# Performance work log

Measured on AMD Instinct MI355X. Metric: run time of the kernel, lower is better.

Reference implementation:

```python
import jax, jax.numpy as jnp
import numpy as np

EPS = 1e-12  # tf.nn.l2_normalize epsilon used inside keras CosineSimilarity


def _cos(a, b):
    # keras CosineSimilarity returns -cos; callers negate explicitly.
    an = a / jnp.sqrt(jnp.maximum(jnp.sum(a * a, axis=-1, keepdims=True), EPS))
    bn = b / jnp.sqrt(jnp.maximum(jnp.sum(b * b, axis=-1, keepdims=True), EPS))
    return jnp.sum(an * bn, axis=-1)


def setup_inputs() -> dict:
    key = jax.random.key(0)
    B, S, D, H, N = 1024, 200, 128, 128, 64
    ks = jax.random.split(key, 8)
    X_series = jax.random.normal(ks[0], (B, S, D), jnp.float32)
    pos_series = jax.random.normal(ks[1], (S, D), jnp.float32)
    X_item = jax.random.normal(ks[2], (B, D), jnp.float32)
    origin = jax.random.normal(ks[3], (B, N, D), jnp.float32)  # X_negative
    # contiguous-prefix validity mask (module assumes valid positions form a prefix)
    lengths = jax.random.randint(ks[4], (B,), 1, S + 1)
    valid_mask = jnp.arange(S)[None, :] < lengths[:, None]
    # learned params (GlorotUniform-scale init)
    Wp = jax.random.normal(ks[5], (D, H), jnp.float32) * 0.08
    We = jax.random.normal(ks[6], (D, H), jnp.float32) * 0.08
    z = jax.random.normal(ks[7], (H,), jnp.float32) * 0.1
    return {"X_series": X_series, "pos_series": pos_series, "X_item": X_item,
            "valid_mask": valid_mask, "origin": origin, "Wp": Wp, "We": We, "z": z}


def reference(X_series, pos_series, X_item, valid_mask, origin, Wp, We, z):
    B, S, D = X_series.shape
    # additive tanh attention: z . tanh(X_series @ We + pos_series @ Wp)
    hidden = jnp.tanh(jnp.einsum('bsd,dh->bsh', X_series, We) + (pos_series @ Wp)[None])
    scores = jnp.einsum('bsh,h->bs', hidden, z)
    scores = jnp.where(valid_mask, scores, -jnp.inf)
    attn = jax.nn.softmax(scores, axis=-1)                      # [B,S]
    attentioned = attn[:, :, None] * X_series                    # [B,S,D]
    attention_output = jnp.sum(attentioned, axis=1)              # [B,D]
    inner = jnp.sum(attention_output * X_item, axis=-1, keepdims=True)
    concated = jnp.concatenate([attention_output, inner], axis=1)  # [B,D+1]

    # ---- auxiliary loss ----
    last_idx = jnp.sum(valid_mask.astype(jnp.int32), axis=1) - 1
    last_vec = attentioned[jnp.arange(B), last_idx]              # gather_nd
    new_mask = (jnp.arange(S)[None, :] < last_idx[:, None]).astype(X_series.dtype)
    out_vec = jnp.sum(attentioned * new_mask[:, :, None], axis=1)  # [B,D]
    # keras CosineSimilarity = -cos_sim; then mapped to (x+1)/2 and used as logits
    pos_logits = (-_cos(last_vec, out_vec) + 1.0) / 2.0          # [B]
    neg_logits = (-_cos(origin, out_vec[:, None, :]) + 1.0) / 2.0  # [B,N]
    pos_loss = jax.nn.softplus(-pos_logits)  # sigmoid_xent labels=1
    neg_loss = jax.nn.softplus(neg_logits)   # sigmoid_xent labels=0
    # NB: TF reduces pos_loss over its only axis -> scalar, broadcast-added to [B]
    auxiliary_loss = jnp.sum(pos_loss) + jnp.sum(neg_loss, axis=-1)  # [B]
    return concated, auxiliary_loss
```

## Files before the change

### kernel.cpp

```cpp
#include <hip/hip_runtime.h>
#include <hip/hip_bf16.h>
#include <math.h>

#define B_ 1024
#define S_ 200
#define D_ 128
#define H_ 128
#define N_ 64

typedef __attribute__((ext_vector_type(8))) short short8;
typedef __attribute__((ext_vector_type(8))) __bf16 bf16x8;
typedef __attribute__((ext_vector_type(4))) float floatx4;

static __device__ __forceinline__ float bf2f(unsigned short u) {
    union { unsigned int i; float f; } v; v.i = ((unsigned int)u) << 16; return v.f;
}
static __device__ __forceinline__ unsigned short f2bf(float f) {
    union { float f; unsigned int u; } v; v.f = f;
    unsigned int u = v.u;
    return (unsigned short)((u + 0x7FFFu + ((u >> 16) & 1u)) >> 16);
}
static __device__ __forceinline__ float ld1(const void* p, int isbf, size_t i) {
    return isbf ? bf2f(((const unsigned short*)p)[i]) : ((const float*)p)[i];
}
static __device__ __forceinline__ float fast_tanh(float x) {
    float t = __expf(2.0f * x);
    return 1.0f - 2.0f * __builtin_amdgcn_rcpf(t + 1.0f);
}

__global__ __launch_bounds__(64) void detect_kernel(
    const void* a0, const void* a1, const void* a2, const void* a3,
    const void* a4, const void* a5, const void* a6, const void* a7,
    int* flags)
{
    int bid = blockIdx.x, t = threadIdx.x;
    if (bid == 3) {
        const unsigned char* mb = (const unsigned char*)a3;
        int f = 0;
        for (int i = t; i < 4096; i += 64)
            if ((i & 3) && mb[i]) f = 1;
        for (int off = 32; off; off >>= 1) f |= __shfl_xor(f, off, 64);
        if (t == 0) flags[3] = f;
        return;
    }
    const void* ptrs[8] = {a0, a1, a2, a3, a4, a5, a6, a7};
    const int counts[8] = {B_*S_*D_, S_*D_, B_*D_, 0, B_*N_*D_, D_*H_, D_*H_, H_};
    const unsigned int* w = (const unsigned int*)ptrs[bid];
    int words = counts[bid] / 2; if (words > 1024) words = 1024;
    int pass = 0, tot = 0;
    for (int i = t; i < words; i += 64) {
        unsigned int e = (w[i] >> 7) & 0xFF;
        tot++;
        if (e == 0 || (e >= 96 && e <= 140)) pass++;
    }
    for (int off = 32; off; off >>= 1) {
        pass += __shfl_xor(pass, off, 64);
        tot  += __shfl_xor(tot,  off, 64);
    }
    if (t == 0) flags[bid] = (pass * 4 >= tot * 3) ? 1 : 0;
}

__global__ __launch_bounds__(256) void lengths_kernel(
    const void* __restrict__ maskv, const int* __restrict__ flags,
    int* __restrict__ lengths)
{
    int wv = threadIdx.x >> 6, lane = threadIdx.x & 63;
    int fMk = flags[3];
    int base = blockIdx.x * 64 + wv * 16;
    for (int bb = 0; bb < 16; ++bb) {
        int b = base + bb;
        int nz = 0;
        if (fMk) {
            const unsigned char* mb = (const unsigned char*)maskv + (size_t)b * S_;
            for (int i = lane; i < S_; i += 64) nz += (mb[i] != 0);
        } else {
            const int* mi = (const int*)maskv + (size_t)b * S_;
            for (int i = lane; i < S_; i += 64) nz += (mi[i] != 0);
        }
        for (int off = 32; off; off >>= 1) nz += __shfl_xor(nz, off, 64);
        if (lane == 0) lengths[b] = nz;
    }
}

__global__ __launch_bounds__(128) void prep_kernel(
    const void* __restrict__ We, const void* __restrict__ pos,
    const void* __restrict__ Wp, const int* __restrict__ flags,
    unsigned short* __restrict__ WeTf, float* __restrict__ pb)
{
    int blk = blockIdx.x, t = threadIdx.x;
    __shared__ unsigned short T[128][136];
    __shared__ float prow[D_];
    if (blk == 0) {
        int fWe = flags[6];
        for (int c = t; c < 2048; c += 128) {
            int d = c >> 4, h8 = (c & 15) * 8;
            short8 v;
            if (fWe) {
                v = *(const short8*)((const unsigned short*)We + d * H_ + h8);
            } else {
                const float* p = (const float*)We + d * H_ + h8;
                float4 a = ((const float4*)p)[0], b = ((const float4*)p)[1];
                v[0] = (short)f2bf(a.x); v[1] = (short)f2bf(a.y);
                v[2] = (short)f2bf(a.z); v[3] = (short)f2bf(a.w);
                v[4] = (short)f2bf(b.x); v[5] = (short)f2bf(b.y);
                v[6] = (short)f2bf(b.z); v[7] = (short)f2bf(b.w);
            }
            *(short8*)(&T[d][h8]) = v;
        }
        __syncthreads();
        for (int i = t; i < 2048; i += 128) {
            int frag = i >> 6, ln = i & 63;
            int nt = frag >> 2, kks = frag & 3;
            int h = nt * 16 + (ln & 15);
            int dbase = kks * 32 + (ln >> 4) * 8;
            short8 v;
#pragma unroll
            for (int j = 0; j < 8; ++j) v[j] = (short)T[dbase + j][h];
            *(short8*)(WeTf + (size_t)i * 8) = v;
        }
    } else {
        int s = blk - 1, h = t;
        prow[h] = ld1(pos, flags[1], (size_t)s * D_ + h);
        __syncthreads();
        float acc = 0.f;
        if (flags[5]) {
            const unsigned short* W = (const unsigned short*)Wp;
            for (int d = 0; d < D_; ++d) acc = fmaf(prow[d], bf2f(W[d * H_ + h]), acc);
        } else {
            const float* W = (const float*)Wp;
            for (int d = 0; d < D_; ++d) acc = fmaf(prow[d], W[d * H_ + h], acc);
        }
        pb[s * H_ + h] = acc;
    }
}

__global__ __launch_bounds__(256) void scores_kernel(
    const void* __restrict__ Xs, const unsigned short* __restrict__ WeTf,
    const void* __restrict__ zv, const float* __restrict__ pb,
    const int* __restrict__ flags, const int* __restrict__ lengths,
    float* __restrict__ scores)
{
    __shared__ unsigned short Bsh[16384];
    int t = threadIdx.x;
    int lane = t & 63, w = t >> 6;
    int quad = lane >> 4, mrow = lane & 15;
    int fXs = flags[0], fz = flags[7];
    int row0 = blockIdx.x * 128 + w * 32;

    for (int i = t; i < 2048; i += 256)
        *(short8*)(Bsh + i * 8) = *(const short8*)(WeTf + (size_t)i * 8);

    float zl[8];
#pragma unroll
    for (int nt = 0; nt < 8; ++nt) zl[nt] = ld1(zv, fz, nt * 16 + mrow);
    __syncthreads();

#pragma unroll
    for (int mt = 0; mt < 2; ++mt) {
        int r = row0 + mt * 16 + mrow;
        int bidx = r / S_, s_ = r - bidx * S_;
        bool valid = s_ < lengths[bidx];
        if (!__any(valid)) continue;

        floatx4 acc[8];
#pragma unroll
        for (int nt = 0; nt < 8; ++nt) {
            acc[nt][0] = 0.f; acc[nt][1] = 0.f; acc[nt][2] = 0.f; acc[nt][3] = 0.f;
        }
#pragma unroll
        for (int kks = 0; kks < 4; ++kks) {
            bf16x8 af;
            size_t roff = (size_t)r * D_ + kks * 32 + quad * 8;
            if (fXs) {
                short8 v = *(const short8*)((const unsigned short*)Xs + roff);
                af = __builtin_bit_cast(bf16x8, v);
            } else {
                const float* p = (const float*)Xs + roff;
                float4 a = ((const float4*)p)[0], b = ((const float4*)p)[1];
                short8 v;
                v[0] = (short)f2bf(a.x); v[1] = (short)f2bf(a.y);
                v[2] = (short)f2bf(a.z); v[3] = (short)f2bf(a.w);
                v[4] = (short)f2bf(b.x); v[5] = (short)f2bf(b.y);
                v[6] = (short)f2bf(b.z); v[7] = (short)f2bf(b.w);
                af = __builtin_bit_cast(bf16x8, v);
            }
#pragma unroll
            for (int nt = 0; nt < 8; ++nt) {
                short8 bv = *(const short8*)(Bsh + (((nt << 2) + kks) * 64 + lane) * 8);
                bf16x8 bf = __builtin_bit_cast(bf16x8, bv);
                acc[nt] = __builtin_amdgcn_mfma_f32_16x16x32_bf16(af, bf, acc[nt], 0, 0, 0);
            }
        }
#pragma unroll
        for (int reg = 0; reg < 4; ++reg) {
            int grow = row0 + mt * 16 + quad * 4 + reg;
            int s = grow % S_;
            const float* pbrow = pb + (size_t)s * H_;
            float rs = 0.f;
#pragma unroll
            for (int nt = 0; nt < 8; ++nt)
                rs = fmaf(fast_tanh(acc[nt][reg] + pbrow[nt * 16 + mrow]), zl[nt], rs);
#pragma unroll
            for (int off = 1; off < 16; off <<= 1)
                rs += __shfl_xor(rs, off, 64);
            if (mrow == 0) scores[grow] = rs;
        }
    }
}

__global__ __launch_bounds__(256) void attnout_kernel(
    const void* __restrict__ Xs, const void* __restrict__ Xitem,
    const void* __restrict__ origin, const float* __restrict__ scores,
    const int* __restrict__ flags, const int* __restrict__ lengths,
    float* __restrict__ pos_loss, float* __restrict__ neg_sum,
    float* __restrict__ out)
{
    int b = blockIdx.x, t = threadIdx.x;
    int wv = t >> 6, lane = t & 63;
    int fXs = flags[0], fXi = flags[2], fOr = flags[4];
    __shared__ float attn[256];
    __shared__ float att_out[D_];
    __shared__ float lastv[D_];
    __shared__ float outv[D_];
    __shared__ float partial[8][D_];
    __shared__ float p_oo[4][64];
    __shared__ float p_ov[4][64];
    __shared__ float red[16];
    __shared__ float sc1s, sc2s, vvs;

    int nn = t >> 2, part = t & 3;
    float o_f[32];
    if (fOr) {
        const unsigned short* p = (const unsigned short*)origin + ((size_t)b * N_ + nn) * D_ + part * 32;
#pragma unroll
        for (int j = 0; j < 4; ++j) {
            uint4 u = *(const uint4*)(p + j * 8);
            o_f[j*8+0] = bf2f((unsigned short)(u.x & 0xffff));
            o_f[j*8+1] = bf2f((unsigned short)(u.x >> 16));
            o_f[j*8+2] = bf2f((unsigned short)(u.y & 0xffff));
            o_f[j*8+3] = bf2f((unsigned short)(u.y >> 16));
            o_f[j*8+4] = bf2f((unsigned short)(u.z & 0xffff));
            o_f[j*8+5] = bf2f((unsigned short)(u.z >> 16));
            o_f[j*8+6] = bf2f((unsigned short)(u.w & 0xffff));
            o_f[j*8+7] = bf2f((unsigned short)(u.w >> 16));
        }
    } else {
        const float* p = (const float*)origin + ((size_t)b * N_ + nn) * D_ + part * 32;
#pragma unroll
        for (int j = 0; j < 8; ++j) {
            float4 v = *(const float4*)(p + j * 4);
            o_f[j*4+0] = v.x; o_f[j*4+1] = v.y; o_f[j*4+2] = v.z; o_f[j*4+3] = v.w;
        }
    }

    int length = lengths[b];
    int last = length - 1;

    float sc = (t < length) ? scores[(size_t)b * S_ + t] : -INFINITY;
    float m = sc;
    for (int off = 32; off; off >>= 1) m = fmaxf(m, __shfl_xor(m, off, 64));
    if (lane == 0) red[wv] = m;
    __syncthreads();
    if (t == 0) sc1s = fmaxf(fmaxf(red[0], red[1]), fmaxf(red[2], red[3]));
    __syncthreads();
    float e = (t < length) ? expf(sc - sc1s) : 0.f;
    float r = e;
    for (int off = 32; off; off >>= 1) r += __shfl_xor(r, off, 64);
    __syncthreads();
    if (lane == 0) red[wv] = r;
    __syncthreads();
    if (t == 0) sc2s = red[0] + red[1] + red[2] + red[3];
    __syncthreads();
    attn[t] = e / sc2s;
    __syncthreads();

    {
        int sp = t >> 5;
        int d4 = (t & 31) * 4;
        float a0 = 0, a1 = 0, a2 = 0, a3 = 0;
        if (fXs) {
#pragma unroll 5
            for (int s = sp; s < length; s += 8) {
                float ww = attn[s];
                uint2 u = *(const uint2*)((const unsigned short*)Xs + ((size_t)b * S_ + s) * D_ + d4);
                a0 = fmaf(ww, bf2f((unsigned short)(u.x & 0xffff)), a0);
                a1 = fmaf(ww, bf2f((unsigned short)(u.x >> 16)), a1);
                a2 = fmaf(ww, bf2f((unsigned short)(u.y & 0xffff)), a2);
                a3 = fmaf(ww, bf2f((unsigned short)(u.y >> 16)), a3);
            }
        } else {
#pragma unroll 5
            for (int s = sp; s < length; s += 8) {
                float ww = attn[s];
                float4 u = *(const float4*)((const float*)Xs + ((size_t)b * S_ + s) * D_ + d4);
                a0 = fmaf(ww, u.x, a0);
                a1 = fmaf(ww, u.y, a1);
                a2 = fmaf(ww, u.z, a2);
                a3 = fmaf(ww, u.w, a3);
            }
        }
        partial[sp][d4] = a0; partial[sp][d4 + 1] = a1;
        partial[sp][d4 + 2] = a2; partial[sp][d4 + 3] = a3;
    }
    __syncthreads();
    if (t < D_) {
        float v = 0.f;
#pragma unroll
        for (int p = 0; p < 8; ++p) v += partial[p][t];
        att_out[t] = v;
        float lv = attn[last] * ld1(Xs, fXs, ((size_t)b * S_ + last) * D_ + t);
        lastv[t] = lv;
        outv[t] = v - lv;
    }
    __syncthreads();

    {
        float pi = (t < D_) ? att_out[t] * ld1(Xitem, fXi, (size_t)b * D_ + t) : 0.f;
        for (int off = 32; off; off >>= 1) pi += __shfl_xor(pi, off, 64);
        if (lane == 0) red[wv] = pi;
        __syncthreads();
        if (t < D_) out[(size_t)b * (D_ + 1) + t] = att_out[t];
        if (t == 0)
            out[(size_t)b * (D_ + 1) + D_] = red[0] + red[1] + red[2] + red[3];
        __syncthreads();
    }

    {
        float l_ = (t < D_) ? lastv[t] : 0.f;
        float o_ = (t < D_) ? outv[t] : 0.f;
        float r0 = l_ * l_, r1 = l_ * o_, r2 = o_ * o_;
        for (int off = 32; off; off >>= 1) {
            r0 += __shfl_xor(r0, off, 64);
            r1 += __shfl_xor(r1, off, 64);
            r2 += __shfl_xor(r2, off, 64);
        }
        if (lane == 0) { red[wv] = r0; red[4 + wv] = r1; red[8 + wv] = r2; }
        __syncthreads();
        if (t == 0) {
            float ll = red[0] + red[1] + red[2] + red[3];
            float lo = red[4] + red[5] + red[6] + red[7];
            float oo = red[8] + red[9] + red[10] + red[11];
            float cosv = lo / (sqrtf(fmaxf(ll, 1e-12f)) * sqrtf(fmaxf(oo, 1e-12f)));
            float pl = 0.5f * (1.f - cosv);
            pos_loss[b] = log1pf(expf(-pl));
            vvs = oo;
        }
        __syncthreads();
    }

    {
        float o_oo = 0.f, o_ov = 0.f;
#pragma unroll
        for (int jj = 0; jj < 32; ++jj) {
            int j = (jj + part * 8) & 31;
            float wv_ = outv[part * 32 + j];
            o_oo = fmaf(o_f[j], o_f[j], o_oo);
            o_ov = fmaf(o_f[j], wv_, o_ov);
        }
        p_oo[part][nn] = o_oo;
        p_ov[part][nn] = o_ov;
        __syncthreads();
        if (t < 64) {
            float oo = p_oo[0][t] + p_oo[1][t] + p_oo[2][t] + p_oo[3][t];
            float ov = p_ov[0][t] + p_ov[1][t] + p_ov[2][t] + p_ov[3][t];
            float cosn = ov / (sqrtf(fmaxf(oo, 1e-12f)) * sqrtf(fmaxf(vvs, 1e-12f)));
            float nl = 0.5f * (1.f - cosn);
            float nloss = log1pf(expf(nl));
            for (int off = 32; off; off >>= 1) nloss += __shfl_xor(nloss, off, 64);
            if (t == 0) neg_sum[b] = nloss;
        }
    }
}

__global__ __launch_bounds__(1024) void final_kernel(
    const float* __restrict__ pos_loss,
    const float* __restrict__ neg_sum,
    float* __restrict__ out)
{
    __shared__ float red[16];
    int t = threadIdx.x;
    float v = pos_loss[t];
    for (int off = 32; off; off >>= 1) v += __shfl_xor(v, off, 64);
    if ((t & 63) == 0) red[t >> 6] = v;
    __syncthreads();
    if (t == 0) {
        float s = 0.f;
#pragma unroll
        for (int i = 0; i < 16; ++i) s += red[i];
        red[0] = s;
    }
    __syncthreads();
    out[(size_t)B_ * (D_ + 1) + t] = red[0] + neg_sum[t];
}

extern "C" void kernel_launch(void* const* d_in, const int* in_sizes, int n_in,
                              void* d_out, int out_size, void* d_ws, size_t ws_size,
                              hipStream_t stream) {
    const void* Xs     = d_in[0];
    const void* pos    = d_in[1];
    const void* Xitem  = d_in[2];
    const void* mask   = d_in[3];
    const void* origin = d_in[4];
    const void* Wp     = d_in[5];
    const void* We     = d_in[6];
    const void* zv     = d_in[7];

    int*   flags    = (int*)d_ws;
    unsigned short* WeTf = (unsigned short*)((char*)d_ws + 128);
    float* pb       = (float*)((char*)d_ws + 128 + 32768);
    float* scores   = pb + 25600;
    float* pos_loss = scores + 204800;
    float* neg_sum  = pos_loss + B_;
    int*   lengths  = (int*)(neg_sum + B_);
    float* out = (float*)d_out;

    detect_kernel<<<8, 64, 0, stream>>>(Xs, pos, Xitem, mask, origin, Wp, We, zv, flags);
    lengths_kernel<<<16, 256, 0, stream>>>(mask, flags, lengths);
    prep_kernel<<<201, 128, 0, stream>>>(We, pos, Wp, flags, WeTf, pb);
    scores_kernel<<<(B_ * S_) / 128, 256, 0, stream>>>(Xs, WeTf, zv, pb, flags, lengths, scores);
    attnout_kernel<<<B_, 256, 0, stream>>>(Xs, Xitem, origin, scores, flags, lengths,
                                           pos_loss, neg_sum, out);
    final_kernel<<<1, 1024, 0, stream>>>(pos_loss, neg_sum, out);
}
```

Before: 280.9 us.

## Merge detect/lengths/prep kernels and interleave two MFMA row tiles in scores

Fuses the dtype-detect, lengths and prep kernels into one launch. Each block recomputes the flags it needs locally instead of waiting for a separate detect launch. The scores kernel now exits whole blocks early when every row lies past the valid length, before staging weights in LDS. It also issues two independent MFMA accumulator chains per wave so A-loads and MFMAs can overlap. The cost is redundant detection work per block and higher register pressure from doubled accumulators.

```diff
diff --git a/kernel.cpp b/kernel.cpp
--- a/kernel.cpp
+++ b/kernel.cpp
@@ -27,28 +27,9 @@
     float t = __expf(2.0f * x);
     return 1.0f - 2.0f * __builtin_amdgcn_rcpf(t + 1.0f);
 }
-
-__global__ __launch_bounds__(64) void detect_kernel(
-    const void* a0, const void* a1, const void* a2, const void* a3,
-    const void* a4, const void* a5, const void* a6, const void* a7,
-    int* flags)
-{
-    int bid = blockIdx.x, t = threadIdx.x;
-    if (bid == 3) {
-        const unsigned char* mb = (const unsigned char*)a3;
-        int f = 0;
-        for (int i = t; i < 4096; i += 64)
-            if ((i & 3) && mb[i]) f = 1;
-        for (int off = 32; off; off >>= 1) f |= __shfl_xor(f, off, 64);
-        if (t == 0) flags[3] = f;
-        return;
-    }
-    const void* ptrs[8] = {a0, a1, a2, a3, a4, a5, a6, a7};
-    const int counts[8] = {B_*S_*D_, S_*D_, B_*D_, 0, B_*N_*D_, D_*H_, D_*H_, H_};
-    const unsigned int* w = (const unsigned int*)ptrs[bid];
-    int words = counts[bid] / 2; if (words > 1024) words = 1024;
+static __device__ __forceinline__ int detect_bf16_wave(const unsigned int* w, int words, int lane) {
     int pass = 0, tot = 0;
-    for (int i = t; i < words; i += 64) {
+    for (int i = lane; i < words; i += 64) {
         unsigned int e = (w[i] >> 7) & 0xFF;
         tot++;
         if (e == 0 || (e >= 96 && e <= 140)) pass++;
@@ -57,41 +38,78 @@
         pass += __shfl_xor(pass, off, 64);
         tot  += __shfl_xor(tot,  off, 64);
     }
-    if (t == 0) flags[bid] = (pass * 4 >= tot * 3) ? 1 : 0;
-}
-
-__global__ __launch_bounds__(256) void lengths_kernel(
-    const void* __restrict__ maskv, const int* __restrict__ flags,
-    int* __restrict__ lengths)
-{
-    int wv = threadIdx.x >> 6, lane = threadIdx.x & 63;
-    int fMk = flags[3];
-    int base = blockIdx.x * 64 + wv * 16;
-    for (int bb = 0; bb < 16; ++bb) {
-        int b = base + bb;
-        int nz = 0;
-        if (fMk) {
-            const unsigned char* mb = (const unsigned char*)maskv + (size_t)b * S_;
-            for (int i = lane; i < S_; i += 64) nz += (mb[i] != 0);
-        } else {
-            const int* mi = (const int*)maskv + (size_t)b * S_;
-            for (int i = lane; i < S_; i += 64) nz += (mi[i] != 0);
-        }
-        for (int off = 32; off; off >>= 1) nz += __shfl_xor(nz, off, 64);
-        if (lane == 0) lengths[b] = nz;
-    }
-}
-
-__global__ __launch_bounds__(128) void prep_kernel(
-    const void* __restrict__ We, const void* __restrict__ pos,
-    const void* __restrict__ Wp, const int* __restrict__ flags,
-    unsigned short* __restrict__ WeTf, float* __restrict__ pb)
+    return (pass * 4 >= tot * 3) ? 1 : 0;
+}
+
+__global__ __launch_bounds__(128) void prep_all_kernel(
+    const void* __restrict__ Xs, const void* __restrict__ pos,
+    const void* __restrict__ Xitem, const void* __restrict__ maskv,
+    const void* __restrict__ origin, const void* __restrict__ Wp,
+    const void* __restrict__ We, const void* __restrict__ zv,
+    int* __restrict__ flags, unsigned short* __restrict__ WeTf,
+    float* __restrict__ pb, int* __restrict__ lengths)
 {
     int blk = blockIdx.x, t = threadIdx.x;
-    __shared__ unsigned short T[128][136];
-    __shared__ float prow[D_];
-    if (blk == 0) {
-        int fWe = flags[6];
+    int lane = t & 63;
+
+    if (blk < 8) {
+        if (t >= 64) return;
+        if (blk == 3) {
+            const unsigned char* mb = (const unsigned char*)maskv;
+            int f = 0;
+            for (int i = t; i < 4096; i += 64)
+                if ((i & 3) && mb[i]) f = 1;
+            for (int off = 32; off; off >>= 1) f |= __shfl_xor(f, off, 64);
+            if (t == 0) flags[3] = f;
+            return;
+        }
+        const void* ptrs[8] = {Xs, pos, Xitem, maskv, origin, Wp, We, zv};
+        const int counts[8] = {B_*S_*D_, S_*D_, B_*D_, 0, B_*N_*D_, D_*H_, D_*H_, H_};
+        int words = counts[blk] / 2; if (words > 1024) words = 1024;
+        int r = detect_bf16_wave((const unsigned int*)ptrs[blk], words, t);
+        if (t == 0) flags[blk] = r;
+        return;
+    }
+
+    if (blk < 40) {
+        __shared__ int fMk_s;
+        const unsigned char* mb = (const unsigned char*)maskv;
+        if (t < 64) {
+            int f = 0;
+            for (int i = t; i < 4096; i += 64)
+                if ((i & 3) && mb[i]) f = 1;
+            for (int off = 32; off; off >>= 1) f |= __shfl_xor(f, off, 64);
+            if (t == 0) fMk_s = f;
+        }
+        __syncthreads();
+        int fMk = fMk_s;
+        int wv = t >> 6;
+        int base = (blk - 8) * 32 + wv * 16;
+        for (int bb = 0; bb < 16; ++bb) {
+            int b = base + bb;
+            int nz = 0;
+            if (fMk) {
+                const unsigned char* mp = mb + (size_t)b * S_;
+                for (int i = lane; i < S_; i += 64) nz += (mp[i] != 0);
+            } else {
+                const int* mi = (const int*)maskv + (size_t)b * S_;
+                for (int i = lane; i < S_; i += 64) nz += (mi[i] != 0);
+            }
+            for (int off = 32; off; off >>= 1) nz += __shfl_xor(nz, off, 64);
+            if (lane == 0) lengths[b] = nz;
+        }
+        return;
+    }
+
+    if (blk == 40) {
+        __shared__ unsigned short T[128][136];
+        __shared__ int fWe_s;
+        if (t < 64) {
+            int r = detect_bf16_wave((const unsigned int*)We, 1024, t);
+            if (t == 0) fWe_s = r;
+        }
+        __syncthreads();
+        int fWe = fWe_s;
         for (int c = t; c < 2048; c += 128) {
             int d = c >> 4, h8 = (c & 15) * 8;
             short8 v;
@@ -118,12 +136,23 @@
             for (int j = 0; j < 8; ++j) v[j] = (short)T[dbase + j][h];
             *(short8*)(WeTf + (size_t)i * 8) = v;
         }
-    } else {
-        int s = blk - 1, h = t;
-        prow[h] = ld1(pos, flags[1], (size_t)s * D_ + h);
+        return;
+    }
+
+    {
+        __shared__ float prow[D_];
+        __shared__ int f2[2];
+        if (t < 64) {
+            int rp = detect_bf16_wave((const unsigned int*)pos, 1024, t);
+            int rw = detect_bf16_wave((const unsigned int*)Wp, 1024, t);
+            if (t == 0) { f2[0] = rp; f2[1] = rw; }
+        }
+        __syncthreads();
+        int s = blk - 41, h = t;
+        prow[h] = ld1(pos, f2[0], (size_t)s * D_ + h);
         __syncthreads();
         float acc = 0.f;
-        if (flags[5]) {
+        if (f2[1]) {
             const unsigned short* W = (const unsigned short*)Wp;
             for (int d = 0; d < D_; ++d) acc = fmaf(prow[d], bf2f(W[d * H_ + h]), acc);
         } else {
@@ -145,7 +174,13 @@
     int lane = t & 63, w = t >> 6;
     int quad = lane >> 4, mrow = lane & 15;
     int fXs = flags[0], fz = flags[7];
-    int row0 = blockIdx.x * 128 + w * 32;
+    int rb = blockIdx.x * 128;
+
+    {
+        int bidx = rb / S_, s0 = rb - bidx * S_;
+        bool crosses = (s0 + 127 >= S_);
+        if (!crosses && s0 >= lengths[bidx]) return;
+    }
 
     for (int i = t; i < 2048; i += 256)
         *(short8*)(Bsh + i * 8) = *(const short8*)(WeTf + (size_t)i * 8);
@@ -155,56 +190,88 @@
     for (int nt = 0; nt < 8; ++nt) zl[nt] = ld1(zv, fz, nt * 16 + mrow);
     __syncthreads();
 
+    int row0 = rb + w * 32;
+    bool v[2];
 #pragma unroll
     for (int mt = 0; mt < 2; ++mt) {
-        int r = row0 + mt * 16 + mrow;
-        int bidx = r / S_, s_ = r - bidx * S_;
-        bool valid = s_ < lengths[bidx];
-        if (!__any(valid)) continue;
-
-        floatx4 acc[8];
-#pragma unroll
-        for (int nt = 0; nt < 8; ++nt) {
-            acc[nt][0] = 0.f; acc[nt][1] = 0.f; acc[nt][2] = 0.f; acc[nt][3] = 0.f;
-        }
+        int rf = row0 + mt * 16;
+        int bidx = rf / S_, s0 = rf - bidx * S_;
+        v[mt] = (s0 + 15 >= S_) || (s0 < lengths[bidx]);
+    }
+    if (!v[0] && !v[1]) return;
+
+    floatx4 accA[8], accB[8];
+#pragma unroll
+    for (int nt = 0; nt < 8; ++nt) {
+        accA[nt][0] = 0.f; accA[nt][1] = 0.f; accA[nt][2] = 0.f; accA[nt][3] = 0.f;
+        accB[nt][0] = 0.f; accB[nt][1] = 0.f; accB[nt][2] = 0.f; accB[nt][3] = 0.f;
+    }
+
+    auto loadA = [&](int r, int kks) -> bf16x8 {
+        size_t roff = (size_t)r * D_ + kks * 32 + quad * 8;
+        if (fXs) {
+            short8 vv = *(const short8*)((const unsigned short*)Xs + roff);
+            return __builtin_bit_cast(bf16x8, vv);
+        }
+        const float* p = (const float*)Xs + roff;
+        float4 a = ((const float4*)p)[0], b = ((const float4*)p)[1];
+        short8 vv;
+        vv[0] = (short)f2bf(a.x); vv[1] = (short)f2bf(a.y);
+        vv[2] = (short)f2bf(a.z); vv[3] = (short)f2bf(a.w);
+        vv[4] = (short)f2bf(b.x); vv[5] = (short)f2bf(b.y);
+        vv[6] = (short)f2bf(b.z); vv[7] = (short)f2bf(b.w);
+        return __builtin_bit_cast(bf16x8, vv);
+    };
+
+    int mtv = v[0] ? 0 : 1;
+    if (v[0] && v[1]) {
+        int r0 = row0 + mrow, r1 = row0 + 16 + mrow;
 #pragma unroll
         for (int kks = 0; kks < 4; ++kks) {
-            bf16x8 af;
-            size_t roff = (size_t)r * D_ + kks * 32 + quad * 8;
-            if (fXs) {
-                short8 v = *(const short8*)((const unsigned short*)Xs + roff);
-                af = __builtin_bit_cast(bf16x8, v);
-            } else {
-                const float* p = (const float*)Xs + roff;
-                float4 a = ((const float4*)p)[0], b = ((const float4*)p)[1];
-                short8 v;
-                v[0] = (short)f2bf(a.x); v[1] = (short)f2bf(a.y);
-                v[2] = (short)f2bf(a.z); v[3] = (short)f2bf(a.w);
-                v[4] = (short)f2bf(b.x); v[5] = (short)f2bf(b.y);
-                v[6] = (short)f2bf(b.z); v[7] = (short)f2bf(b.w);
-                af = __builtin_bit_cast(bf16x8, v);
-            }
+            bf16x8 a0 = loadA(r0, kks), a1 = loadA(r1, kks);
 #pragma unroll
             for (int nt = 0; nt < 8; ++nt) {
                 short8 bv = *(const short8*)(Bsh + (((nt << 2) + kks) * 64 + lane) * 8);
                 bf16x8 bf = __builtin_bit_cast(bf16x8, bv);
-                acc[nt] = __builtin_amdgcn_mfma_f32_16x16x32_bf16(af, bf, acc[nt], 0, 0, 0);
-            }
-        }
+                accA[nt] = __builtin_amdgcn_mfma_f32_16x16x32_bf16(a0, bf, accA[nt], 0, 0, 0);
+                accB[nt] = __builtin_amdgcn_mfma_f32_16x16x32_bf16(a1, bf, accB[nt], 0, 0, 0);
+            }
+        }
+    } else {
+        int r0 = row0 + mtv * 16 + mrow;
+#pragma unroll
+        for (int kks = 0; kks < 4; ++kks) {
+            bf16x8 a0 = loadA(r0, kks);
+#pragma unroll
+            for (int nt = 0; nt < 8; ++nt) {
+                short8 bv = *(const short8*)(Bsh + (((nt << 2) + kks) * 64 + lane) * 8);
+                bf16x8 bf = __builtin_bit_cast(bf16x8, bv);
+                accA[nt] = __builtin_amdgcn_mfma_f32_16x16x32_bf16(a0, bf, accA[nt], 0, 0, 0);
+            }
+        }
+    }
+
+    auto epilogue = [&](const floatx4* acc8, int rowbase) {
 #pragma unroll
         for (int reg = 0; reg < 4; ++reg) {
-            int grow = row0 + mt * 16 + quad * 4 + reg;
+            int grow = rowbase + quad * 4 + reg;
             int s = grow % S_;
             const float* pbrow = pb + (size_t)s * H_;
             float rs = 0.f;
 #pragma unroll
             for (int nt = 0; nt < 8; ++nt)
-                rs = fmaf(fast_tanh(acc[nt][reg] + pbrow[nt * 16 + mrow]), zl[nt], rs);
+                rs = fmaf(fast_tanh(acc8[nt][reg] + pbrow[nt * 16 + mrow]), zl[nt], rs);
 #pragma unroll
             for (int off = 1; off < 16; off <<= 1)
                 rs += __shfl_xor(rs, off, 64);
             if (mrow == 0) scores[grow] = rs;
         }
+    };
+    if (v[0] && v[1]) {
+        epilogue(accA, row0);
+        epilogue(accB, row0 + 16);
+    } else {
+        epilogue(accA, row0 + mtv * 16);
     }
 }
 
@@ -414,9 +481,8 @@
     int*   lengths  = (int*)(neg_sum + B_);
     float* out = (float*)d_out;
 
-    detect_kernel<<<8, 64, 0, stream>>>(Xs, pos, Xitem, mask, origin, Wp, We, zv, flags);
-    lengths_kernel<<<16, 256, 0, stream>>>(mask, flags, lengths);
-    prep_kernel<<<201, 128, 0, stream>>>(We, pos, Wp, flags, WeTf, pb);
+    prep_all_kernel<<<241, 128, 0, stream>>>(Xs, pos, Xitem, mask, origin, Wp, We, zv,
+                                             flags, WeTf, pb, lengths);
     scores_kernel<<<(B_ * S_) / 128, 256, 0, stream>>>(Xs, WeTf, zv, pb, flags, lengths, scores);
     attnout_kernel<<<B_, 256, 0, stream>>>(Xs, Xitem, origin, scores, flags, lengths,
                                            pos_loss, neg_sum, out);
```

New measurement: 274.0 us. 2.4% less time.
